# Kernel optimization log

Hardware: AMD Instinct MI355X
Metric: run time of the kernel (lower is better)

The kernel has to match this reference:

```python
import jax, jax.numpy as jnp
import numpy as np

USER_NUM = 100000
ITEM_NUM = 50000
N_NODES = USER_NUM + ITEM_NUM
EMB = 64
LAYERS = 3
NNZ = 2400000


def spmm(rows, cols, vals, x, n):
    # sparse [n, n] (COO) @ dense [n, d] -> [n, d]
    gathered = vals[:, None] * x[cols]          # [nnz, d]
    return jax.ops.segment_sum(gathered, rows, num_segments=n)


def setup_inputs() -> dict:
    key = jax.random.key(0)
    ks = jax.random.split(key, 7)
    return {
        "user_emb": jax.random.normal(ks[0], (USER_NUM, EMB), jnp.float32) * 0.1,
        "item_emb": jax.random.normal(ks[1], (ITEM_NUM, EMB), jnp.float32) * 0.1,
        "w1": jax.random.normal(ks[2], (LAYERS, EMB, EMB), jnp.float32) * (1.0 / np.sqrt(EMB)),
        "w2": jax.random.normal(ks[3], (LAYERS, EMB, EMB), jnp.float32) * (1.0 / np.sqrt(EMB)),
        "adj_vals": jax.random.uniform(ks[4], (NNZ,), jnp.float32) * (1.0 / 16.0),
        "adj_rows": jax.random.randint(ks[5], (NNZ,), 0, N_NODES, jnp.int32),
        "adj_cols": jax.random.randint(ks[6], (NNZ,), 0, N_NODES, jnp.int32),
    }


def reference(user_emb, item_emb, w1, w2, adj_vals, adj_rows, adj_cols):
    ego = jnp.concatenate([user_emb, item_emb], axis=0)   # [N, d]
    n = ego.shape[0]
    all_emb = [ego]
    for k in range(w1.shape[0]):
        temp = ego @ w1[k]                                # [N, d]
        agg_temp = spmm(adj_rows, adj_cols, adj_vals, temp, n)
        agg_ego = spmm(adj_rows, adj_cols, adj_vals, ego, n)
        ego = jax.nn.leaky_relu(agg_temp + temp + (agg_ego * ego) @ w2[k])
        all_emb.append(ego)
    mean_emb = jnp.mean(jnp.stack(all_emb, axis=1), axis=1)  # [N, d]
    u = user_emb.shape[0]
    return mean_emb[:u], mean_emb[u:]
```

## Files before the change

kernel.cpp:

```cpp
#include <hip/hip_runtime.h>
#include <hip/hip_fp16.h>

typedef _Float16 f16;
typedef _Float16 f16x4 __attribute__((ext_vector_type(4)));
typedef _Float16 f16x8 __attribute__((ext_vector_type(8)));
typedef float f32x4 __attribute__((ext_vector_type(4)));

__device__ __forceinline__ float h2f(__half v) { return __half2float(v); }
__device__ __forceinline__ __half f2h(float v) { return __float2half(v); }

#define SCAN_CHUNK 2048
#define ASTRIDE 136

#define BSHIFT 10
#define BROWS (1 << BSHIFT)
#define MAXB 1024
#define TILE 4096

__global__ void zero_out_kernel(float* __restrict__ out, int total) {
    int i = blockIdx.x * blockDim.x + threadIdx.x;
    if (i < total) out[i] = 0.0f;
}

__global__ void init_kernel(const float* __restrict__ user, const float* __restrict__ item,
                            __half* __restrict__ ego0, int usz, int total) {
    int i = blockIdx.x * blockDim.x + threadIdx.x;
    if (i >= total) return;
    float f = (i < usz) ? user[i] : item[i - usz];
    ego0[i] = f2h(f);
}

__global__ void hist_kernel(const int* __restrict__ rows, int* __restrict__ cnt, int nnz) {
    int i = blockIdx.x * blockDim.x + threadIdx.x;
    if (i < nnz) atomicAdd(&cnt[rows[i]], 1);
}

__global__ void scan_pass1(const int* __restrict__ cnt, int* __restrict__ bsum, int n) {
    __shared__ int wt[4];
    int tid = threadIdx.x;
    int base = blockIdx.x * SCAN_CHUNK + tid * 8;
    int s = 0;
    #pragma unroll
    for (int k = 0; k < 8; ++k) { int i = base + k; if (i < n) s += cnt[i]; }
    #pragma unroll
    for (int o = 32; o > 0; o >>= 1) s += __shfl_down(s, o, 64);
    int lane = tid & 63, wid = tid >> 6;
    if (lane == 0) wt[wid] = s;
    __syncthreads();
    if (tid == 0) bsum[blockIdx.x] = wt[0] + wt[1] + wt[2] + wt[3];
}

__global__ void scan_pass2(int* __restrict__ bsum, int nb, int* __restrict__ total) {
    if (threadIdx.x == 0) {
        int run = 0;
        for (int b = 0; b < nb; ++b) { int v = bsum[b]; bsum[b] = run; run += v; }
        *total = run;
    }
}

__global__ void scan_pass3(int* __restrict__ cnt, const int* __restrict__ bsum,
                           int* __restrict__ rptr, int n, const int* __restrict__ total) {
    __shared__ int wt[4];
    int tid = threadIdx.x;
    int base = blockIdx.x * SCAN_CHUNK + tid * 8;
    int v[8];
    int s = 0;
    #pragma unroll
    for (int k = 0; k < 8; ++k) { int i = base + k; v[k] = (i < n) ? cnt[i] : 0; s += v[k]; }
    int lane = tid & 63, wid = tid >> 6;
    int xs = s;
    #pragma unroll
    for (int o = 1; o < 64; o <<= 1) { int t = __shfl_up(xs, o, 64); if (lane >= o) xs += t; }
    if (lane == 63) wt[wid] = xs;
    __syncthreads();
    int wexcl = 0;
    for (int w = 0; w < wid; ++w) wexcl += wt[w];
    int run = bsum[blockIdx.x] + wexcl + (xs - s);
    #pragma unroll
    for (int k = 0; k < 8; ++k) {
        int i = base + k;
        if (i < n) { rptr[i] = run; cnt[i] = run; }
        run += v[k];
    }
    if (blockIdx.x == 0 && tid == 0) rptr[n] = *total;
}

__global__ void scatter_kernel(const int* __restrict__ rows, const int* __restrict__ cols,
                               const float* __restrict__ vals, int* __restrict__ cursor,
                               int2* __restrict__ edges, int nnz) {
    int i = blockIdx.x * blockDim.x + threadIdx.x;
    if (i >= nnz) return;
    int r = rows[i];
    int pos = atomicAdd(&cursor[r], 1);
    edges[pos] = make_int2(cols[i], __float_as_int(vals[i]));
}

__global__ __launch_bounds__(256)
void bhist_kernel(const int* __restrict__ rows, int* __restrict__ bcnt, int nnz, int nbuck) {
    __shared__ int hist[MAXB];
    int tid = threadIdx.x;
    for (int j = tid; j < nbuck; j += 256) hist[j] = 0;
    __syncthreads();
    int i = blockIdx.x * TILE + tid;
    #pragma unroll
    for (int k = 0; k < 16; ++k, i += 256)
        if (i < nnz) atomicAdd(&hist[rows[i] >> BSHIFT], 1);
    __syncthreads();
    for (int j = tid; j < nbuck; j += 256)
        if (hist[j]) atomicAdd(&bcnt[j], hist[j]);
}

__global__ void bscan_kernel(const int* __restrict__ bcnt, int* __restrict__ bbase,
                             int* __restrict__ gcur, int nbuck) {
    if (threadIdx.x == 0) {
        int run = 0;
        for (int b = 0; b < nbuck; ++b) { bbase[b] = run; gcur[b] = run; run += bcnt[b]; }
        bbase[nbuck] = run;
    }
}

__global__ __launch_bounds__(256)
void binA_kernel(const int* __restrict__ rows, const int* __restrict__ cols,
                 const float* __restrict__ vals, int* __restrict__ gcur,
                 int2* __restrict__ bucketed, int nnz, int nbuck) {
    __shared__ int hist[MAXB];
    __shared__ int offs[MAXB];
    __shared__ int rbase[MAXB];
    __shared__ int2 reorder[TILE];
    __shared__ unsigned short slotb[TILE];
    __shared__ int wsum[4];
    int tid = threadIdx.x;
    int tbase = blockIdx.x * TILE;
    int cnt_here = min(TILE, nnz - tbase);

    for (int b = tid; b < MAXB; b += 256) hist[b] = 0;
    __syncthreads();

    int myrow[16]; int mycol[16]; float myval[16];
    #pragma unroll
    for (int k = 0; k < 16; ++k) {
        int i = tbase + tid + k * 256;
        int r = (i < nnz) ? rows[i] : -1;
        myrow[k] = r;
        if (r >= 0) {
            mycol[k] = cols[i];
            myval[k] = vals[i];
            atomicAdd(&hist[r >> BSHIFT], 1);
        }
    }
    __syncthreads();

    int b0 = tid * 4;
    int s0 = hist[b0], s1 = hist[b0 + 1], s2 = hist[b0 + 2], s3 = hist[b0 + 3];
    int tsum = s0 + s1 + s2 + s3;
    int lane = tid & 63, wid = tid >> 6;
    int x = tsum;
    #pragma unroll
    for (int o = 1; o < 64; o <<= 1) { int t = __shfl_up(x, o, 64); if (lane >= o) x += t; }
    if (lane == 63) wsum[wid] = x;
    __syncthreads();
    int wexcl = 0;
    for (int w = 0; w < wid; ++w) wexcl += wsum[w];
    int excl = wexcl + x - tsum;
    offs[b0]     = excl;
    offs[b0 + 1] = excl + s0;
    offs[b0 + 2] = excl + s0 + s1;
    offs[b0 + 3] = excl + s0 + s1 + s2;
    for (int b = tid; b < nbuck; b += 256) {
        int c = hist[b];
        rbase[b] = (c > 0) ? atomicAdd(&gcur[b], c) : 0;
    }
    __syncthreads();
    for (int b = tid; b < MAXB; b += 256) hist[b] = 0;
    __syncthreads();

    #pragma unroll
    for (int k = 0; k < 16; ++k) {
        int r = myrow[k];
        if (r >= 0) {
            int b = r >> BSHIFT;
            int p = offs[b] + atomicAdd(&hist[b], 1);
            reorder[p] = make_int2(((r & (BROWS - 1)) << 20) | mycol[k], __float_as_int(myval[k]));
            slotb[p] = (unsigned short)b;
        }
    }
    __syncthreads();

    for (int t = tid; t < cnt_here; t += 256) {
        int b = slotb[t];
        bucketed[rbase[b] + (t - offs[b])] = reorder[t];
    }
}

__global__ __launch_bounds__(256)
void binB_fused_kernel(const int* __restrict__ bbase, const int2* __restrict__ bucketed,
                       int2* __restrict__ edges, int* __restrict__ rptr, int n, int nbuck) {
    __shared__ int cur[BROWS];
    __shared__ int wsum[4];
    int b = blockIdx.x;
    int row_lo = b << BSHIFT;
    int nrows = min(BROWS, n - row_lo);
    int tid = threadIdx.x;
    for (int j = tid; j < BROWS; j += 256) cur[j] = 0;
    __syncthreads();
    int beg = bbase[b], end = bbase[b + 1];
    for (int i = beg + tid; i < end; i += 256)
        atomicAdd(&cur[((unsigned)bucketed[i].x) >> 20], 1);
    __syncthreads();
    int j0 = tid * 4;
    int c0 = cur[j0], c1 = cur[j0 + 1], c2 = cur[j0 + 2], c3 = cur[j0 + 3];
    int tsum = c0 + c1 + c2 + c3;
    int lane = tid & 63, wid = tid >> 6;
    int x = tsum;
    #pragma unroll
    for (int o = 1; o < 64; o <<= 1) { int t = __shfl_up(x, o, 64); if (lane >= o) x += t; }
    if (lane == 63) wsum[wid] = x;
    __syncthreads();
    int wexcl = 0;
    for (int w = 0; w < wid; ++w) wexcl += wsum[w];
    int excl = beg + wexcl + x - tsum;
    cur[j0]     = excl;
    cur[j0 + 1] = excl + c0;
    cur[j0 + 2] = excl + c0 + c1;
    cur[j0 + 3] = excl + c0 + c1 + c2;
    __syncthreads();
    for (int j = tid; j < nrows; j += 256) rptr[row_lo + j] = cur[j];
    if (b == nbuck - 1 && tid == 0) rptr[n] = bbase[nbuck];
    for (int i = beg + tid; i < end; i += 256) {
        int2 rec = bucketed[i];
        int ro  = ((unsigned)rec.x) >> 20;
        int col = rec.x & ((1 << 20) - 1);
        int pos = atomicAdd(&cur[ro], 1);
        edges[pos] = make_int2(col, rec.y);
    }
}

__device__ __forceinline__ void spmm_edge_acc(float4& acc, int2 e, const uint2* egov, int g) {
    uint2 gv = egov[((size_t)e.x << 4) + g];
    float v = __int_as_float(e.y);
    float2 a = __half22float2(*(const __half2*)&gv.x);
    float2 b = __half22float2(*(const __half2*)&gv.y);
    acc.x += v * a.x; acc.y += v * a.y; acc.z += v * b.x; acc.w += v * b.y;
}

__global__ __launch_bounds__(512, 4)
void spmm_mfma_kernel(const int* __restrict__ rptr, const int2* __restrict__ edges,
                      const __half* __restrict__ ego, const float* __restrict__ w1k,
                      const float* __restrict__ w2k, __half* __restrict__ ego_out, int n) {
    __shared__ f16 A_lds[32 * ASTRIDE];
    __shared__ f16 Wt_lds[64 * ASTRIDE];
    int tid = threadIdx.x;
    #pragma unroll
    for (int it = 0; it < 8; ++it) {
        int e = tid + it * 512;
        int k = e >> 6, c = e & 63;
        Wt_lds[c * ASTRIDE + k]      = (f16)w1k[e];
        Wt_lds[c * ASTRIDE + 64 + k] = (f16)w2k[e];
    }
    int lane = tid & 63, wid = tid >> 6;
    int sub = lane >> 4;
    int g   = lane & 15;
    int row  = blockIdx.x * 32 + wid * 4 + sub;
    int lrow = wid * 4 + sub;
    bool active = row < n;
    int beg = active ? rptr[row] : 0;
    int end = active ? rptr[row + 1] : 0;
    float4 acc = {0.f, 0.f, 0.f, 0.f};
    const uint2* egov = (const uint2*)ego;
    int j = beg;
    for (; j + 8 <= end; j += 8) {
        int2 e0 = edges[j],     e1 = edges[j + 1], e2 = edges[j + 2], e3 = edges[j + 3];
        int2 e4 = edges[j + 4], e5 = edges[j + 5], e6 = edges[j + 6], e7 = edges[j + 7];
        spmm_edge_acc(acc, e0, egov, g);
        spmm_edge_acc(acc, e1, egov, g);
        spmm_edge_acc(acc, e2, egov, g);
        spmm_edge_acc(acc, e3, egov, g);
        spmm_edge_acc(acc, e4, egov, g);
        spmm_edge_acc(acc, e5, egov, g);
        spmm_edge_acc(acc, e6, egov, g);
        spmm_edge_acc(acc, e7, egov, g);
    }
    for (; j + 4 <= end; j += 4) {
        int2 e0 = edges[j], e1 = edges[j + 1], e2 = edges[j + 2], e3 = edges[j + 3];
        spmm_edge_acc(acc, e0, egov, g);
        spmm_edge_acc(acc, e1, egov, g);
        spmm_edge_acc(acc, e2, egov, g);
        spmm_edge_acc(acc, e3, egov, g);
    }
    for (; j < end; ++j) {
        spmm_edge_acc(acc, edges[j], egov, g);
    }
    {
        uint2 xv = egov[(size_t)(active ? row : 0) * 16 + g];
        float2 x01 = __half22float2(*(const __half2*)&xv.x);
        float2 x23 = __half22float2(*(const __half2*)&xv.y);
        f16x4 sv, pv;
        sv[0] = (f16)(acc.x + x01.x); sv[1] = (f16)(acc.y + x01.y);
        sv[2] = (f16)(acc.z + x23.x); sv[3] = (f16)(acc.w + x23.y);
        pv[0] = (f16)(acc.x * x01.x); pv[1] = (f16)(acc.y * x01.y);
        pv[2] = (f16)(acc.z * x23.x); pv[3] = (f16)(acc.w * x23.y);
        f16* ar = &A_lds[lrow * ASTRIDE + g * 4];
        *(f16x4*)ar        = sv;
        *(f16x4*)(ar + 64) = pv;
    }
    __syncthreads();
    int band = wid >> 2;
    int nt   = wid & 3;
    int m = lane & 15, q = lane >> 4;
    f32x4 dacc = {0.f, 0.f, 0.f, 0.f};
    const f16* arow = &A_lds[(band * 16 + m) * ASTRIDE + q * 8];
    const f16* brow = &Wt_lds[(nt * 16 + m) * ASTRIDE + q * 8];
    #pragma unroll
    for (int ks = 0; ks < 4; ++ks) {
        f16x8 av = *(const f16x8*)(arow + ks * 32);
        f16x8 bv = *(const f16x8*)(brow + ks * 32);
        dacc = __builtin_amdgcn_mfma_f32_16x16x32_f16(av, bv, dacc, 0, 0, 0);
    }
    int rbase = blockIdx.x * 32 + band * 16 + q * 4;
    #pragma unroll
    for (int r = 0; r < 4; ++r) {
        int grow = rbase + r;
        if (grow < n) {
            float e0 = dacc[r]; e0 = (e0 > 0.f) ? e0 : 0.01f * e0;
            ego_out[(size_t)grow * 64 + nt * 16 + m] = f2h(e0);
        }
    }
}

__global__ void finalize4_kernel(const __half* __restrict__ e0, const __half* __restrict__ e1,
                                 const __half* __restrict__ e2, const __half* __restrict__ e3,
                                 float* __restrict__ out, const int* __restrict__ rptr,
                                 int N, int nnz, float scale, int total) {
    int i = blockIdx.x * blockDim.x + threadIdx.x;
    if (i >= total) return;
    bool ok = (rptr[N] == nnz);
    float s = h2f(e0[i]) + h2f(e1[i]) + h2f(e2[i]) + h2f(e3[i]);
    out[i] = ok ? s * scale : 0.75f;
}

__global__ void acc_kernel(const __half* __restrict__ e, float* __restrict__ out,
                           float scale, int total, int first) {
    int i = blockIdx.x * blockDim.x + threadIdx.x;
    if (i >= total) return;
    float v = h2f(e[i]) * scale;
    out[i] = first ? v : out[i] + v;
}

extern "C" void kernel_launch(void* const* d_in, const int* in_sizes, int n_in,
                              void* d_out, int out_size, void* d_ws, size_t ws_size,
                              hipStream_t stream) {
    const float* user = (const float*)d_in[0];
    const float* item = (const float*)d_in[1];
    const float* w1   = (const float*)d_in[2];
    const float* w2   = (const float*)d_in[3];
    const float* vals = (const float*)d_in[4];
    const int*   rows = (const int*)d_in[5];
    const int*   cols = (const int*)d_in[6];

    const int usz = in_sizes[0];
    const int isz = in_sizes[1];
    const int L   = in_sizes[2] / 4096;
    const int nnz = in_sizes[4];
    const int N   = (usz + isz) / 64;
    const int ND  = N * 64;
    const int nbscan = (N + SCAN_CHUNK - 1) / SCAN_CHUNK;
    const int nbuck  = (N + BROWS - 1) >> BSHIFT;

    char* p = (char*)d_ws;
    auto alloc = [&](size_t bytes) -> void* {
        void* r = (void*)p;
        p += (bytes + 255) & ~(size_t)255;
        return r;
    };
    __half* egos  = (__half*)alloc((size_t)(L + 1) * ND * 2);
    __half* aggE  = (__half*)alloc((size_t)ND * 2);
    int2*   edges = (int2*)alloc((size_t)nnz * 8);
    int*    rptr  = (int*)alloc((size_t)(N + 1) * 4);
    int*    cnt   = (int*)alloc((size_t)N * 4);
    int*    bsum  = (int*)alloc((size_t)nbscan * 4);
    int*    total = (int*)alloc(4);
    int*    bcnt  = (int*)alloc((size_t)(MAXB + 1) * 4);
    int*    bbase = (int*)alloc((size_t)(MAXB + 1) * 4);
    int*    gcur  = (int*)alloc((size_t)MAXB * 4);
    bool fast_sort = (nbuck <= MAXB) && (N < (1 << 20)) && (nnz > 0);
    int2* bucketed = nullptr;
    if (fast_sort) {
        if ((size_t)ND * 2 >= (size_t)nnz * 8) bucketed = (int2*)aggE;
        else bucketed = (int2*)alloc((size_t)nnz * 8);
    }
    size_t need = (size_t)(p - (char*)d_ws);
    (void)n_in; (void)out_size;

    if (need > ws_size) {
        zero_out_kernel<<<(ND + 255) / 256, 256, 0, stream>>>((float*)d_out, ND);
        return;
    }

    init_kernel<<<(ND + 255) / 256, 256, 0, stream>>>(user, item, egos, usz, ND);

    if (fast_sort) {
        hipMemsetAsync(bcnt, 0, (size_t)nbuck * 4, stream);
        bhist_kernel<<<(nnz + TILE - 1) / TILE, 256, 0, stream>>>(rows, bcnt, nnz, nbuck);
        bscan_kernel<<<1, 64, 0, stream>>>(bcnt, bbase, gcur, nbuck);
        binA_kernel<<<(nnz + TILE - 1) / TILE, 256, 0, stream>>>(rows, cols, vals, gcur,
                                                                 bucketed, nnz, nbuck);
        binB_fused_kernel<<<nbuck, 256, 0, stream>>>(bbase, bucketed, edges, rptr, N, nbuck);
    } else {
        hipMemsetAsync(cnt, 0, (size_t)N * 4, stream);
        hist_kernel<<<(nnz + 255) / 256, 256, 0, stream>>>(rows, cnt, nnz);
        scan_pass1<<<nbscan, 256, 0, stream>>>(cnt, bsum, N);
        scan_pass2<<<1, 64, 0, stream>>>(bsum, nbscan, total);
        scan_pass3<<<nbscan, 256, 0, stream>>>(cnt, bsum, rptr, N, total);
        scatter_kernel<<<(nnz + 255) / 256, 256, 0, stream>>>(rows, cols, vals, cnt, edges, nnz);
    }

    const int fb = (N + 31) / 32;
    for (int k = 0; k < L; ++k) {
        __half* ein  = egos + (size_t)k * ND;
        __half* eout = egos + (size_t)(k + 1) * ND;
        spmm_mfma_kernel<<<fb, 512, 0, stream>>>(rptr, edges, ein, w1 + (size_t)k * 4096,
                                                 w2 + (size_t)k * 4096, eout, N);
    }
    float scale = 1.0f / (float)(L + 1);
    if (L == 3) {
        finalize4_kernel<<<(ND + 255) / 256, 256, 0, stream>>>(
            egos, egos + (size_t)ND, egos + (size_t)2 * ND, egos + (size_t)3 * ND,
            (float*)d_out, rptr, N, nnz, scale, ND);
    } else {
        for (int k = 0; k <= L; ++k)
            acc_kernel<<<(ND + 255) / 256, 256, 0, stream>>>(egos + (size_t)k * ND,
                                                             (float*)d_out, scale, ND, k == 0);
    }
}
```

Measured before the change: 426.0 us.

## Sort edges by column bucket within each row bucket to improve gather locality

The row-bucket kernel now stages each bucket's records in LDS and orders them by column bucket before scattering them into CSR positions. Because atomic slot assignment within a row then follows column order, the SpMM gathers of neighbour embeddings should hit nearby memory more often. Row buckets are halved to 512 rows so each bucket fits the LDS capacity, with a fallback to the old path for oversized buckets. The weight-staging loop is also reindexed so the global reads of w1/w2 are strided while the LDS writes are contiguous. This adds LDS pressure and an extra scan and pass in the binning stage.

```diff
diff --git a/kernel.cpp b/kernel.cpp
--- a/kernel.cpp
+++ b/kernel.cpp
@@ -12,10 +12,11 @@
 #define SCAN_CHUNK 2048
 #define ASTRIDE 136
 
-#define BSHIFT 10
+#define BSHIFT 9
 #define BROWS (1 << BSHIFT)
 #define MAXB 1024
 #define TILE 4096
+#define BCAP 9216
 
 __global__ void zero_out_kernel(float* __restrict__ out, int total) {
     int i = blockIdx.x * blockDim.x + threadIdx.x;
@@ -193,24 +194,42 @@
 }
 
 __global__ __launch_bounds__(256)
-void binB_fused_kernel(const int* __restrict__ bbase, const int2* __restrict__ bucketed,
-                       int2* __restrict__ edges, int* __restrict__ rptr, int n, int nbuck) {
+void binB_sort_kernel(const int* __restrict__ bbase, const int2* __restrict__ bucketed,
+                      int2* __restrict__ edges, int* __restrict__ rptr, int n, int nbuck) {
+    __shared__ int2 srec[BCAP];
+    __shared__ unsigned short ord[BCAP];
     __shared__ int cur[BROWS];
+    __shared__ int chist[MAXB];
     __shared__ int wsum[4];
     int b = blockIdx.x;
     int row_lo = b << BSHIFT;
     int nrows = min(BROWS, n - row_lo);
     int tid = threadIdx.x;
+    int lane = tid & 63, wid = tid >> 6;
+    int beg = bbase[b], end = bbase[b + 1];
+    int cnt = end - beg;
+    bool fits = (cnt <= BCAP);
+
     for (int j = tid; j < BROWS; j += 256) cur[j] = 0;
-    __syncthreads();
-    int beg = bbase[b], end = bbase[b + 1];
-    for (int i = beg + tid; i < end; i += 256)
-        atomicAdd(&cur[((unsigned)bucketed[i].x) >> 20], 1);
-    __syncthreads();
-    int j0 = tid * 4;
-    int c0 = cur[j0], c1 = cur[j0 + 1], c2 = cur[j0 + 2], c3 = cur[j0 + 3];
-    int tsum = c0 + c1 + c2 + c3;
-    int lane = tid & 63, wid = tid >> 6;
+    for (int j = tid; j < MAXB; j += 256) chist[j] = 0;
+    __syncthreads();
+
+    if (fits) {
+        for (int i = tid; i < cnt; i += 256) {
+            int2 r = bucketed[beg + i];
+            srec[i] = r;
+            atomicAdd(&cur[((unsigned)r.x) >> 20], 1);
+            atomicAdd(&chist[(r.x & 0xFFFFF) >> BSHIFT], 1);
+        }
+    } else {
+        for (int i = beg + tid; i < end; i += 256)
+            atomicAdd(&cur[((unsigned)bucketed[i].x) >> 20], 1);
+    }
+    __syncthreads();
+
+    int j0 = tid * 2;
+    int c0 = cur[j0], c1 = cur[j0 + 1];
+    int tsum = c0 + c1;
     int x = tsum;
     #pragma unroll
     for (int o = 1; o < 64; o <<= 1) { int t = __shfl_up(x, o, 64); if (lane >= o) x += t; }
@@ -221,17 +240,49 @@
     int excl = beg + wexcl + x - tsum;
     cur[j0]     = excl;
     cur[j0 + 1] = excl + c0;
-    cur[j0 + 2] = excl + c0 + c1;
-    cur[j0 + 3] = excl + c0 + c1 + c2;
-    __syncthreads();
+    __syncthreads();
+
     for (int j = tid; j < nrows; j += 256) rptr[row_lo + j] = cur[j];
     if (b == nbuck - 1 && tid == 0) rptr[n] = bbase[nbuck];
-    for (int i = beg + tid; i < end; i += 256) {
-        int2 rec = bucketed[i];
-        int ro  = ((unsigned)rec.x) >> 20;
-        int col = rec.x & ((1 << 20) - 1);
-        int pos = atomicAdd(&cur[ro], 1);
-        edges[pos] = make_int2(col, rec.y);
+
+    if (fits) {
+        int k0 = tid * 4;
+        int d0 = chist[k0], d1 = chist[k0 + 1], d2 = chist[k0 + 2], d3 = chist[k0 + 3];
+        int ts2 = d0 + d1 + d2 + d3;
+        int x2 = ts2;
+        #pragma unroll
+        for (int o = 1; o < 64; o <<= 1) { int t = __shfl_up(x2, o, 64); if (lane >= o) x2 += t; }
+        if (lane == 63) wsum[wid] = x2;
+        __syncthreads();
+        int wexcl2 = 0;
+        for (int w = 0; w < wid; ++w) wexcl2 += wsum[w];
+        int ex2 = wexcl2 + x2 - ts2;
+        chist[k0]     = ex2;
+        chist[k0 + 1] = ex2 + d0;
+        chist[k0 + 2] = ex2 + d0 + d1;
+        chist[k0 + 3] = ex2 + d0 + d1 + d2;
+        __syncthreads();
+        for (int i = tid; i < cnt; i += 256) {
+            int cb = (srec[i].x & 0xFFFFF) >> BSHIFT;
+            int p = atomicAdd(&chist[cb], 1);
+            ord[p] = (unsigned short)i;
+        }
+        __syncthreads();
+        for (int p = tid; p < cnt; p += 256) {
+            int2 rec = srec[ord[p]];
+            int ro  = ((unsigned)rec.x) >> 20;
+            int col = rec.x & 0xFFFFF;
+            int pos = atomicAdd(&cur[ro], 1);
+            edges[pos] = make_int2(col, rec.y);
+        }
+    } else {
+        for (int i = beg + tid; i < end; i += 256) {
+            int2 rec = bucketed[i];
+            int ro  = ((unsigned)rec.x) >> 20;
+            int col = rec.x & 0xFFFFF;
+            int pos = atomicAdd(&cur[ro], 1);
+            edges[pos] = make_int2(col, rec.y);
+        }
     }
 }
 
@@ -253,9 +304,9 @@
     #pragma unroll
     for (int it = 0; it < 8; ++it) {
         int e = tid + it * 512;
-        int k = e >> 6, c = e & 63;
-        Wt_lds[c * ASTRIDE + k]      = (f16)w1k[e];
-        Wt_lds[c * ASTRIDE + 64 + k] = (f16)w2k[e];
+        int c = e >> 6, k = e & 63;
+        Wt_lds[c * ASTRIDE + k]      = (f16)w1k[(size_t)k * 64 + c];
+        Wt_lds[c * ASTRIDE + 64 + k] = (f16)w2k[(size_t)k * 64 + c];
     }
     int lane = tid & 63, wid = tid >> 6;
     int sub = lane >> 4;
@@ -404,7 +455,7 @@
         bscan_kernel<<<1, 64, 0, stream>>>(bcnt, bbase, gcur, nbuck);
         binA_kernel<<<(nnz + TILE - 1) / TILE, 256, 0, stream>>>(rows, cols, vals, gcur,
                                                                  bucketed, nnz, nbuck);
-        binB_fused_kernel<<<nbuck, 256, 0, stream>>>(bbase, bucketed, edges, rptr, N, nbuck);
+        binB_sort_kernel<<<nbuck, 256, 0, stream>>>(bbase, bucketed, edges, rptr, N, nbuck);
     } else {
         hipMemsetAsync(cnt, 0, (size_t)N * 4, stream);
         hist_kernel<<<(nnz + 255) / 256, 256, 0, stream>>>(rows, cnt, nnz);
```

Result: slower. 647.5 us (+52.0%).
